# Optimization experiments

Measured on AMD Instinct MI355X. Metric: run time of the kernel, lower is better.

Reference implementation:

```python
import jax, jax.numpy as jnp
import numpy as np
import math

B, N, C, H, CH = 1, 256, 128, 4, 32  # batch, n_res, pair channels, heads, head dim
LN_EPS = 1e-5


def setup_inputs() -> dict:
    key = jax.random.key(0)
    ks = jax.random.split(key, 12)
    s = 0.02
    return {
        "act": jax.random.normal(ks[0], (B, N, N, C), dtype=jnp.float32),
        "mask": (jax.random.uniform(ks[1], (B, N, N)) < 0.9).astype(jnp.float32),
        "ln_g": jnp.ones((C,), jnp.float32),
        "ln_b": jnp.zeros((C,), jnp.float32),
        "wq": jax.random.normal(ks[2], (C, H * CH), jnp.float32) * s,
        "wk": jax.random.normal(ks[3], (C, H * CH), jnp.float32) * s,
        "wv": jax.random.normal(ks[4], (C, H * CH), jnp.float32) * s,
        "w2d": jax.random.normal(ks[5], (C, H), jnp.float32) * s,
        "wg": jax.random.normal(ks[6], (C, H * CH), jnp.float32) * s,
        "bg": jnp.ones((H * CH,), jnp.float32),
        "wo": jax.random.normal(ks[7], (H * CH, C), jnp.float32) * s,
        "bo": jnp.zeros((C,), jnp.float32),
    }


def reference(act, mask, ln_g, ln_b, wq, wk, wv, w2d, wg, bg, wo, bo):
    # swap the two residue axes: attend along the *starting* node axis
    x = jnp.swapaxes(act, -2, -3)          # [b, m, i, C]
    m = jnp.swapaxes(mask, -1, -2)         # [b, m, i]
    # LayerNorm
    mu = jnp.mean(x, axis=-1, keepdims=True)
    var = jnp.var(x, axis=-1, keepdims=True)
    x = (x - mu) * jax.lax.rsqrt(var + LN_EPS) * ln_g + ln_b
    # additive mask bias: [b, m, 1, 1, i]
    bias = (1e9 * (m - 1.0))[..., :, None, None, :]
    shp = x.shape[:-1]
    q = (x @ wq).reshape(*shp, H, CH)
    k = (x @ wk).reshape(*shp, H, CH)
    v = (x @ wv).reshape(*shp, H, CH)
    factor = 1.0 / math.sqrt(CH)
    aff = jnp.einsum('bmihc,bmjhc->bmhij', q * factor, k) + bias
    # non-batched pair bias: [b, h, m, i]; broadcasts against [b, m, h, i, j]
    # exactly as in the torch code (requires b == 1)
    nb = jnp.transpose(x @ w2d, (0, 3, 1, 2))
    weights = jax.nn.softmax(aff + nb, axis=-1)  # [b, m, h, i, j]
    g = jax.nn.sigmoid((x @ wg + bg).reshape(*shp, H, CH))
    out = jnp.einsum('bmhqk,bmkhc->bmqhc', weights, v) * g
    out = out.reshape(*shp, H * CH) @ wo + bo
    return jnp.swapaxes(out, -2, -3)
```

## Files before the change

### kernel.cpp

```cpp
#include <hip/hip_runtime.h>
#include <hip/hip_bf16.h>
#include <math.h>


typedef __attribute__((ext_vector_type(8))) short short8;
typedef __attribute__((ext_vector_type(4))) short short4v;
typedef __attribute__((ext_vector_type(4))) float f32x4;

__device__ __forceinline__ unsigned short f2bf(float f) {
  __hip_bfloat16 b = __float2bfloat16(f);
  return __builtin_bit_cast(unsigned short, b);
}
__device__ __forceinline__ float bf2f(unsigned short u) {
  return __uint_as_float(((unsigned int)u) << 16);
}

__device__ __forceinline__ f32x4 mfma16(short8 a, short8 b, f32x4 c) {
  return __builtin_amdgcn_mfma_f32_16x16x32_bf16(a, b, c, 0, 0, 0);
}

__global__ __launch_bounds__(256) void k_ln(const float* __restrict__ act,
                                            const float* __restrict__ ln_g,
                                            const float* __restrict__ ln_b,
                                            const float* __restrict__ wq,
                                            const float* __restrict__ wk,
                                            const float* __restrict__ wv,
                                            const float* __restrict__ wg,
                                            const float* __restrict__ w2d,
                                            const float* __restrict__ wo,
                                            const float* __restrict__ mask,
                                            unsigned short* __restrict__ lnxb,
                                            unsigned short* __restrict__ Wt4,
                                            unsigned short* __restrict__ Wto,
                                            float* __restrict__ maskT) {
  int t = threadIdx.x;
  if (blockIdx.x >= 4096) {
    int idx = (blockIdx.x - 4096) * 256 + t;
    if (idx < 65536) {
      int n = idx >> 7, k = idx & 127;
      const float* ws = (n < 128) ? wq : (n < 256) ? wk : (n < 384) ? wv : wg;
      Wt4[idx] = f2bf(ws[k * 128 + (n & 127)]);
    } else if (idx < 73728) {
      int j = idx - 65536;
      int r = j >> 7, k = j & 127;
      Wt4[idx] = (r < 4) ? f2bf(w2d[k * 4 + r]) : (unsigned short)0;
    } else if (idx < 90112) {
      int j = idx - 73728;
      int n = j >> 7, k = j & 127;
      Wto[j] = f2bf(wo[k * 128 + n]);
    } else if (idx < 155648) {
      int j2 = idx - 90112;
      int mi = j2 & 255, jj = j2 >> 8;
      maskT[mi * 256 + jj] = 1e9f * (mask[jj * 256 + mi] - 1.0f);
    }
    return;
  }
  int grp = t >> 4, l16 = t & 15;
  int row = blockIdx.x * 16 + grp;
  int mm = row >> 8, ii = row & 255;
  const float4* a = (const float4*)(act + ((size_t)(ii * 256 + mm)) * 128);
  float4 v0 = a[l16 * 2], v1 = a[l16 * 2 + 1];
  float s = (v0.x + v0.y) + (v0.z + v0.w) + (v1.x + v1.y) + (v1.z + v1.w);
  #pragma unroll
  for (int off = 1; off < 16; off <<= 1) s += __shfl_xor(s, off, 64);
  float mean = s * (1.f / 128.f);
  float e[8] = {v0.x - mean, v0.y - mean, v0.z - mean, v0.w - mean,
                v1.x - mean, v1.y - mean, v1.z - mean, v1.w - mean};
  float vs = (e[0]*e[0] + e[1]*e[1]) + (e[2]*e[2] + e[3]*e[3]) +
             (e[4]*e[4] + e[5]*e[5]) + (e[6]*e[6] + e[7]*e[7]);
  #pragma unroll
  for (int off = 1; off < 16; off <<= 1) vs += __shfl_xor(vs, off, 64);
  float rstd = rsqrtf(vs * (1.f / 128.f) + 1e-5f);
  const float4* gp = (const float4*)ln_g;
  const float4* bp = (const float4*)ln_b;
  float4 g0 = gp[l16 * 2], g1 = gp[l16 * 2 + 1];
  float4 b0 = bp[l16 * 2], b1 = bp[l16 * 2 + 1];
  short8 o;
  o[0] = (short)f2bf(e[0] * rstd * g0.x + b0.x);
  o[1] = (short)f2bf(e[1] * rstd * g0.y + b0.y);
  o[2] = (short)f2bf(e[2] * rstd * g0.z + b0.z);
  o[3] = (short)f2bf(e[3] * rstd * g0.w + b0.w);
  o[4] = (short)f2bf(e[4] * rstd * g1.x + b1.x);
  o[5] = (short)f2bf(e[5] * rstd * g1.y + b1.y);
  o[6] = (short)f2bf(e[6] * rstd * g1.z + b1.z);
  o[7] = (short)f2bf(e[7] * rstd * g1.w + b1.w);
  *(short8*)(lnxb + (size_t)row * 128 + l16 * 8) = o;
}

__global__ __launch_bounds__(256) void k_projg(const unsigned short* __restrict__ A,
                                               const unsigned short* __restrict__ Bt,
                                               const float* __restrict__ bg,
                                               unsigned short* __restrict__ qb,
                                               unsigned short* __restrict__ kb,
                                               unsigned short* __restrict__ vb,
                                               unsigned short* __restrict__ sgb,
                                               float* __restrict__ b2t) {
  __shared__ unsigned short As[128 * 40];
  __shared__ unsigned short Bs[64 * 40];
  int t = threadIdx.x;
  int m0 = blockIdx.x * 128, n0 = blockIdx.y * 64;
  int w = t >> 6, l = t & 63, g = l >> 4, li = l & 15;
  int wr = w >> 1, wc = w & 1;
  f32x4 acc[4][2] = {};
  for (int s = 0; s < 4; ++s) {
    int k0 = s * 32;
    __syncthreads();
    {
      int row = t >> 1, kl = (t & 1) * 16;
      const short8* src = (const short8*)(A + (size_t)(m0 + row) * 128 + k0 + kl);
      *(short8*)&As[row * 40 + kl]     = src[0];
      *(short8*)&As[row * 40 + kl + 8] = src[1];
      int bn = t >> 2, bk = (t & 3) * 8;
      *(short8*)&Bs[bn * 40 + bk] = *(const short8*)(Bt + (size_t)(n0 + bn) * 128 + k0 + bk);
    }
    __syncthreads();
    short8 af[4], bf[2];
    #pragma unroll
    for (int it = 0; it < 4; ++it)
      af[it] = *(const short8*)&As[(wr * 64 + it * 16 + li) * 40 + g * 8];
    #pragma unroll
    for (int jt = 0; jt < 2; ++jt)
      bf[jt] = *(const short8*)&Bs[(wc * 32 + jt * 16 + li) * 40 + g * 8];
    #pragma unroll
    for (int it = 0; it < 4; ++it)
      #pragma unroll
      for (int jt = 0; jt < 2; ++jt)
        acc[it][jt] = mfma16(bf[jt], af[it], acc[it][jt]);
  }
  int which = n0 >> 7;
  if (which == 4) {
    if (wc == 0 && g == 0) {
      #pragma unroll
      for (int it = 0; it < 4; ++it) {
        int R = m0 + wr * 64 + it * 16 + li;
        int mm = R >> 8, ii = R & 255;
        #pragma unroll
        for (int r = 0; r < 4; ++r)
          b2t[(size_t)r * 65536 + ii * 256 + mm] = acc[it][0][r];
      }
    }
    return;
  }
  const float factor = 0.17677669529663687f;
  #pragma unroll
  for (int it = 0; it < 4; ++it) {
    int R = m0 + wr * 64 + it * 16 + li;
    int mm = R >> 8, ii = R & 255;
    #pragma unroll
    for (int jt = 0; jt < 2; ++jt) {
      int nb4 = n0 + wc * 32 + jt * 16 + g * 4;
      int hh = (nb4 >> 5) & 3, ch = nb4 & 31;
      size_t o = ((size_t)((mm * 4 + hh) * 256 + ii)) * 32 + ch;
      short4v pk;
      if (which == 0) {
        #pragma unroll
        for (int r = 0; r < 4; ++r) pk[r] = (short)f2bf(acc[it][jt][r] * factor);
        *(short4v*)(qb + o) = pk;
      } else if (which == 1) {
        #pragma unroll
        for (int r = 0; r < 4; ++r) pk[r] = (short)f2bf(acc[it][jt][r]);
        *(short4v*)(kb + o) = pk;
      } else if (which == 2) {
        #pragma unroll
        for (int r = 0; r < 4; ++r) pk[r] = (short)f2bf(acc[it][jt][r]);
        *(short4v*)(vb + o) = pk;
      } else {
        #pragma unroll
        for (int r = 0; r < 4; ++r)
          pk[r] = (short)f2bf(1.f / (1.f + __expf(-(acc[it][jt][r] + bg[(nb4 & 127) + r]))));
        *(short4v*)(sgb + o) = pk;
      }
    }
  }
}

__global__ __launch_bounds__(256) void k_attn(const unsigned short* __restrict__ qb,
                                              const unsigned short* __restrict__ kb,
                                              const unsigned short* __restrict__ vb,
                                              const unsigned short* __restrict__ sgb,
                                              const float* __restrict__ b2t,
                                              const float* __restrict__ maskT,
                                              unsigned short* __restrict__ aob) {
  __shared__ unsigned short VT[32 * 264];
  __shared__ unsigned short Pl[4 * 32 * 72];
  __shared__ float maskls[256];
  int m = blockIdx.x >> 1, ihalf = blockIdx.x & 1, h = blockIdx.y;
  int t = threadIdx.x, w = t >> 6, l = t & 63, g = l >> 4, li = l & 15;
  int base = (m * 4 + h) << 8;
  maskls[t] = maskT[m * 256 + t];
  {
    const unsigned int* v32 = (const unsigned int*)(vb + (size_t)base * 32);
    #pragma unroll
    for (int p = 0; p < 16; ++p) {
      int idx = t + p * 256;
      int j = idx >> 4, cp = idx & 15;
      unsigned int u = v32[idx];
      VT[(cp * 2) * 264 + j]     = (unsigned short)(u & 0xffff);
      VT[(cp * 2 + 1) * 264 + j] = (unsigned short)(u >> 16);
    }
  }
  __syncthreads();
  int i0 = ihalf * 128 + w * 32;
  short8 qf[2];
  #pragma unroll
  for (int it = 0; it < 2; ++it)
    qf[it] = *(const short8*)(qb + ((size_t)(base + i0 + it * 16 + li)) * 32 + g * 8);
  float mst[2] = {-1e30f, -1e30f};
  float lst[2] = {0.f, 0.f};
  f32x4 oacc[2][2] = {};
  const float* b2 = b2t + (size_t)h * 65536;
  unsigned short* Pw = Pl + w * 32 * 72;
  for (int jc = 0; jc < 4; ++jc) {
    int j0 = jc * 64;
    f32x4 sacc[4][2];
    #pragma unroll
    for (int jt = 0; jt < 4; ++jt) {
      short8 kf = *(const short8*)(kb + ((size_t)(base + j0 + jt * 16 + li)) * 32 + g * 8);
      #pragma unroll
      for (int it = 0; it < 2; ++it) {
        f32x4 z = {0.f, 0.f, 0.f, 0.f};
        sacc[jt][it] = mfma16(kf, qf[it], z);
      }
    }
    #pragma unroll
    for (int it = 0; it < 2; ++it) {
      int ic = i0 + it * 16 + li;
      float s[16];
      float cmax = -1e30f;
      #pragma unroll
      for (int jt = 0; jt < 4; ++jt) {
        int jb = j0 + jt * 16 + g * 4;
        f32x4 mk = *(const f32x4*)&maskls[jb];
        #pragma unroll
        for (int r = 0; r < 4; ++r) {
          float sv = sacc[jt][it][r] + b2[(size_t)(jb + r) * 256 + ic] + mk[r];
          s[jt * 4 + r] = sv;
          cmax = fmaxf(cmax, sv);
        }
      }
      cmax = fmaxf(cmax, __shfl_xor(cmax, 16));
      cmax = fmaxf(cmax, __shfl_xor(cmax, 32));
      float mnew = fmaxf(mst[it], cmax);
      float fac = __expf(mst[it] - mnew);
      mst[it] = mnew;
      lst[it] *= fac;
      oacc[0][it] *= fac;
      oacc[1][it] *= fac;
      float psum = 0.f;
      #pragma unroll
      for (int jt = 0; jt < 4; ++jt) {
        float p0 = __expf(s[jt * 4 + 0] - mnew);
        float p1 = __expf(s[jt * 4 + 1] - mnew);
        float p2 = __expf(s[jt * 4 + 2] - mnew);
        float p3 = __expf(s[jt * 4 + 3] - mnew);
        psum += p0 + p1 + p2 + p3;
        short4v pk;
        pk.x = (short)f2bf(p0); pk.y = (short)f2bf(p1);
        pk.z = (short)f2bf(p2); pk.w = (short)f2bf(p3);
        *(short4v*)&Pw[(it * 16 + li) * 72 + jt * 16 + g * 4] = pk;
      }
      lst[it] += psum;
    }
    asm volatile("" ::: "memory");
    #pragma unroll
    for (int ks = 0; ks < 2; ++ks) {
      short8 vf0 = *(const short8*)&VT[li * 264        + j0 + ks * 32 + g * 8];
      short8 vf1 = *(const short8*)&VT[(16 + li) * 264 + j0 + ks * 32 + g * 8];
      #pragma unroll
      for (int it = 0; it < 2; ++it) {
        short8 pf = *(const short8*)&Pw[(it * 16 + li) * 72 + ks * 32 + g * 8];
        oacc[0][it] = mfma16(vf0, pf, oacc[0][it]);
        oacc[1][it] = mfma16(vf1, pf, oacc[1][it]);
      }
    }
    asm volatile("" ::: "memory");
  }
  #pragma unroll
  for (int it = 0; it < 2; ++it) {
    float lt = lst[it];
    lt += __shfl_xor(lt, 16);
    lt += __shfl_xor(lt, 32);
    float inv = 1.f / lt;
    int ic = i0 + it * 16 + li;
    #pragma unroll
    for (int ct = 0; ct < 2; ++ct) {
      int c0 = ct * 16 + g * 4;
      const unsigned short* grow = sgb + ((size_t)(base + ic)) * 32 + c0;
      ushort4 gu = *(const ushort4*)grow;
      ushort4 ov;
      ov.x = f2bf(oacc[ct][it][0] * inv * bf2f(gu.x));
      ov.y = f2bf(oacc[ct][it][1] * inv * bf2f(gu.y));
      ov.z = f2bf(oacc[ct][it][2] * inv * bf2f(gu.z));
      ov.w = f2bf(oacc[ct][it][3] * inv * bf2f(gu.w));
      *(ushort4*)&aob[((size_t)(ic * 256 + m)) * 128 + h * 32 + c0] = ov;
    }
  }
}

__global__ __launch_bounds__(256) void k_outg(const unsigned short* __restrict__ A,
                                              const unsigned short* __restrict__ Bt,
                                              const float* __restrict__ bo,
                                              float* __restrict__ out) {
  __shared__ unsigned short As[128 * 40];
  __shared__ unsigned short Bs[64 * 40];
  int t = threadIdx.x;
  int m0 = blockIdx.x * 128, n0 = blockIdx.y * 64;
  int w = t >> 6, l = t & 63, g = l >> 4, li = l & 15;
  int wr = w >> 1, wc = w & 1;
  f32x4 acc[4][2] = {};
  for (int s = 0; s < 4; ++s) {
    int k0 = s * 32;
    __syncthreads();
    {
      int row = t >> 1, kl = (t & 1) * 16;
      const short8* src = (const short8*)(A + (size_t)(m0 + row) * 128 + k0 + kl);
      *(short8*)&As[row * 40 + kl]     = src[0];
      *(short8*)&As[row * 40 + kl + 8] = src[1];
      int bn = t >> 2, bk = (t & 3) * 8;
      *(short8*)&Bs[bn * 40 + bk] = *(const short8*)(Bt + (size_t)(n0 + bn) * 128 + k0 + bk);
    }
    __syncthreads();
    short8 af[4], bf[2];
    #pragma unroll
    for (int it = 0; it < 4; ++it)
      af[it] = *(const short8*)&As[(wr * 64 + it * 16 + li) * 40 + g * 8];
    #pragma unroll
    for (int jt = 0; jt < 2; ++jt)
      bf[jt] = *(const short8*)&Bs[(wc * 32 + jt * 16 + li) * 40 + g * 8];
    #pragma unroll
    for (int it = 0; it < 4; ++it)
      #pragma unroll
      for (int jt = 0; jt < 2; ++jt)
        acc[it][jt] = mfma16(bf[jt], af[it], acc[it][jt]);
  }
  #pragma unroll
  for (int it = 0; it < 4; ++it) {
    int R = m0 + wr * 64 + it * 16 + li;
    #pragma unroll
    for (int jt = 0; jt < 2; ++jt) {
      int nb4 = n0 + wc * 32 + jt * 16 + g * 4;
      float4 o;
      o.x = acc[it][jt][0] + bo[nb4 + 0];
      o.y = acc[it][jt][1] + bo[nb4 + 1];
      o.z = acc[it][jt][2] + bo[nb4 + 2];
      o.w = acc[it][jt][3] + bo[nb4 + 3];
      *(float4*)(out + (size_t)R * 128 + nb4) = o;
    }
  }
}

extern "C" void kernel_launch(void* const* d_in, const int* in_sizes, int n_in,
                              void* d_out, int out_size, void* d_ws, size_t ws_size,
                              hipStream_t stream) {
  const float* act  = (const float*)d_in[0];
  const float* mask = (const float*)d_in[1];
  const float* ln_g = (const float*)d_in[2];
  const float* ln_b = (const float*)d_in[3];
  const float* wq   = (const float*)d_in[4];
  const float* wk   = (const float*)d_in[5];
  const float* wv   = (const float*)d_in[6];
  const float* w2d  = (const float*)d_in[7];
  const float* wg   = (const float*)d_in[8];
  const float* bg   = (const float*)d_in[9];
  const float* wo   = (const float*)d_in[10];
  const float* bo   = (const float*)d_in[11];

  char* p = (char*)d_ws;
  unsigned short* lnxb  = (unsigned short*)p;  p += (size_t)8388608 * 2;
  float*          b2t   = (float*)p;           p += (size_t)262144 * 4;
  unsigned short* qb    = (unsigned short*)p;  p += (size_t)8388608 * 2;
  unsigned short* kb    = (unsigned short*)p;  p += (size_t)8388608 * 2;
  unsigned short* vb    = (unsigned short*)p;  p += (size_t)8388608 * 2;
  unsigned short* sgb   = (unsigned short*)p;  p += (size_t)8388608 * 2;
  unsigned short* aob   = (unsigned short*)p;  p += (size_t)8388608 * 2;
  unsigned short* Wt4   = (unsigned short*)p;  p += (size_t)73728 * 2;
  unsigned short* Wto   = (unsigned short*)p;  p += (size_t)16384 * 2;
  float*          maskT = (float*)p;           p += (size_t)65536 * 4;
  float* out = (float*)d_out;

  hipLaunchKernelGGL(k_ln,    dim3(4704),   dim3(256), 0, stream,
                     act, ln_g, ln_b, wq, wk, wv, wg, w2d, wo, mask, lnxb, Wt4, Wto, maskT);
  hipLaunchKernelGGL(k_projg, dim3(512, 9), dim3(256), 0, stream, lnxb, Wt4, bg, qb, kb, vb, sgb, b2t);
  hipLaunchKernelGGL(k_attn,  dim3(512, 4), dim3(256), 0, stream, qb, kb, vb, sgb, b2t, maskT, aob);
  hipLaunchKernelGGL(k_outg,  dim3(512, 2), dim3(256), 0, stream, aob, Wto, bo, out);
}
```

Baseline: 95.58 us.

## Write V pre-transposed from projection kernel and read it directly in attention

The projection kernel now computes the V tile with swapped MFMA operands and stores V in a channel-major [m,h,c,j] layout. The attention kernel drops its LDS transpose staging of V and loads V fragments straight from global memory, issuing those loads before the softmax so they overlap it. This removes the per-block LDS transpose, its shared memory and its scalar LDS stores, at the cost of repeated global/L2 reads of V by every wave and narrower strided stores in the projection epilogue.

```diff
diff --git a/kernel.cpp b/kernel.cpp
--- a/kernel.cpp
+++ b/kernel.cpp
@@ -92,7 +92,7 @@
                                                const float* __restrict__ bg,
                                                unsigned short* __restrict__ qb,
                                                unsigned short* __restrict__ kb,
-                                               unsigned short* __restrict__ vb,
+                                               unsigned short* __restrict__ vtb,
                                                unsigned short* __restrict__ sgb,
                                                float* __restrict__ b2t) {
   __shared__ unsigned short As[128 * 40];
@@ -101,6 +101,7 @@
   int m0 = blockIdx.x * 128, n0 = blockIdx.y * 64;
   int w = t >> 6, l = t & 63, g = l >> 4, li = l & 15;
   int wr = w >> 1, wc = w & 1;
+  int which = n0 >> 7;
   f32x4 acc[4][2] = {};
   for (int s = 0; s < 4; ++s) {
     int k0 = s * 32;
@@ -121,13 +122,20 @@
     #pragma unroll
     for (int jt = 0; jt < 2; ++jt)
       bf[jt] = *(const short8*)&Bs[(wc * 32 + jt * 16 + li) * 40 + g * 8];
-    #pragma unroll
-    for (int it = 0; it < 4; ++it)
-      #pragma unroll
-      for (int jt = 0; jt < 2; ++jt)
-        acc[it][jt] = mfma16(bf[jt], af[it], acc[it][jt]);
-  }
-  int which = n0 >> 7;
+    if (which == 2) {
+      #pragma unroll
+      for (int it = 0; it < 4; ++it)
+        #pragma unroll
+        for (int jt = 0; jt < 2; ++jt)
+          acc[it][jt] = mfma16(af[it], bf[jt], acc[it][jt]);
+    } else {
+      #pragma unroll
+      for (int it = 0; it < 4; ++it)
+        #pragma unroll
+        for (int jt = 0; jt < 2; ++jt)
+          acc[it][jt] = mfma16(bf[jt], af[it], acc[it][jt]);
+    }
+  }
   if (which == 4) {
     if (wc == 0 && g == 0) {
       #pragma unroll
@@ -137,6 +145,23 @@
         #pragma unroll
         for (int r = 0; r < 4; ++r)
           b2t[(size_t)r * 65536 + ii * 256 + mm] = acc[it][0][r];
+      }
+    }
+    return;
+  }
+  if (which == 2) {
+    #pragma unroll
+    for (int it = 0; it < 4; ++it) {
+      int R0 = m0 + wr * 64 + it * 16 + g * 4;
+      int mm = R0 >> 8, ii0 = R0 & 255;
+      #pragma unroll
+      for (int jt = 0; jt < 2; ++jt) {
+        int n = n0 + wc * 32 + jt * 16 + li;
+        int hh = (n >> 5) & 3, ch = n & 31;
+        short4v pk;
+        #pragma unroll
+        for (int r = 0; r < 4; ++r) pk[r] = (short)f2bf(acc[it][jt][r]);
+        *(short4v*)(vtb + ((size_t)((mm * 4 + hh) * 32 + ch)) * 256 + ii0) = pk;
       }
     }
     return;
@@ -160,10 +185,6 @@
         #pragma unroll
         for (int r = 0; r < 4; ++r) pk[r] = (short)f2bf(acc[it][jt][r]);
         *(short4v*)(kb + o) = pk;
-      } else if (which == 2) {
-        #pragma unroll
-        for (int r = 0; r < 4; ++r) pk[r] = (short)f2bf(acc[it][jt][r]);
-        *(short4v*)(vb + o) = pk;
       } else {
         #pragma unroll
         for (int r = 0; r < 4; ++r)
@@ -176,30 +197,19 @@
 
 __global__ __launch_bounds__(256) void k_attn(const unsigned short* __restrict__ qb,
                                               const unsigned short* __restrict__ kb,
-                                              const unsigned short* __restrict__ vb,
+                                              const unsigned short* __restrict__ vtb,
                                               const unsigned short* __restrict__ sgb,
                                               const float* __restrict__ b2t,
                                               const float* __restrict__ maskT,
                                               unsigned short* __restrict__ aob) {
-  __shared__ unsigned short VT[32 * 264];
   __shared__ unsigned short Pl[4 * 32 * 72];
   __shared__ float maskls[256];
   int m = blockIdx.x >> 1, ihalf = blockIdx.x & 1, h = blockIdx.y;
   int t = threadIdx.x, w = t >> 6, l = t & 63, g = l >> 4, li = l & 15;
   int base = (m * 4 + h) << 8;
   maskls[t] = maskT[m * 256 + t];
-  {
-    const unsigned int* v32 = (const unsigned int*)(vb + (size_t)base * 32);
-    #pragma unroll
-    for (int p = 0; p < 16; ++p) {
-      int idx = t + p * 256;
-      int j = idx >> 4, cp = idx & 15;
-      unsigned int u = v32[idx];
-      VT[(cp * 2) * 264 + j]     = (unsigned short)(u & 0xffff);
-      VT[(cp * 2 + 1) * 264 + j] = (unsigned short)(u >> 16);
-    }
-  }
   __syncthreads();
+  const unsigned short* vt = vtb + (size_t)base * 32;
   int i0 = ihalf * 128 + w * 32;
   short8 qf[2];
   #pragma unroll
@@ -222,6 +232,12 @@
         sacc[jt][it] = mfma16(kf, qf[it], z);
       }
     }
+    short8 vf[2][2];
+    #pragma unroll
+    for (int ks = 0; ks < 2; ++ks) {
+      vf[ks][0] = *(const short8*)(vt + (size_t)li * 256        + j0 + ks * 32 + g * 8);
+      vf[ks][1] = *(const short8*)(vt + (size_t)(16 + li) * 256 + j0 + ks * 32 + g * 8);
+    }
     #pragma unroll
     for (int it = 0; it < 2; ++it) {
       int ic = i0 + it * 16 + li;
@@ -264,13 +280,11 @@
     asm volatile("" ::: "memory");
     #pragma unroll
     for (int ks = 0; ks < 2; ++ks) {
-      short8 vf0 = *(const short8*)&VT[li * 264        + j0 + ks * 32 + g * 8];
-      short8 vf1 = *(const short8*)&VT[(16 + li) * 264 + j0 + ks * 32 + g * 8];
       #pragma unroll
       for (int it = 0; it < 2; ++it) {
         short8 pf = *(const short8*)&Pw[(it * 16 + li) * 72 + ks * 32 + g * 8];
-        oacc[0][it] = mfma16(vf0, pf, oacc[0][it]);
-        oacc[1][it] = mfma16(vf1, pf, oacc[1][it]);
+        oacc[0][it] = mfma16(vf[ks][0], pf, oacc[0][it]);
+        oacc[1][it] = mfma16(vf[ks][1], pf, oacc[1][it]);
       }
     }
     asm volatile("" ::: "memory");
@@ -370,7 +384,7 @@
   float*          b2t   = (float*)p;           p += (size_t)262144 * 4;
   unsigned short* qb    = (unsigned short*)p;  p += (size_t)8388608 * 2;
   unsigned short* kb    = (unsigned short*)p;  p += (size_t)8388608 * 2;
-  unsigned short* vb    = (unsigned short*)p;  p += (size_t)8388608 * 2;
+  unsigned short* vtb   = (unsigned short*)p;  p += (size_t)8388608 * 2;
   unsigned short* sgb   = (unsigned short*)p;  p += (size_t)8388608 * 2;
   unsigned short* aob   = (unsigned short*)p;  p += (size_t)8388608 * 2;
   unsigned short* Wt4   = (unsigned short*)p;  p += (size_t)73728 * 2;
@@ -380,7 +394,7 @@
 
   hipLaunchKernelGGL(k_ln,    dim3(4704),   dim3(256), 0, stream,
                      act, ln_g, ln_b, wq, wk, wv, wg, w2d, wo, mask, lnxb, Wt4, Wto, maskT);
-  hipLaunchKernelGGL(k_projg, dim3(512, 9), dim3(256), 0, stream, lnxb, Wt4, bg, qb, kb, vb, sgb, b2t);
-  hipLaunchKernelGGL(k_attn,  dim3(512, 4), dim3(256), 0, stream, qb, kb, vb, sgb, b2t, maskT, aob);
+  hipLaunchKernelGGL(k_projg, dim3(512, 9), dim3(256), 0, stream, lnxb, Wt4, bg, qb, kb, vtb, sgb, b2t);
+  hipLaunchKernelGGL(k_attn,  dim3(512, 4), dim3(256), 0, stream, qb, kb, vtb, sgb, b2t, maskT, aob);
   hipLaunchKernelGGL(k_outg,  dim3(512, 2), dim3(256), 0, stream, aob, Wto, bo, out);
 }
```

Result: slower. 123.0 us (+28.7%).
